# Kernel optimization log

Hardware: AMD Instinct MI355X
Metric: run time of the kernel (lower is better)

Reference implementation:

```python
import jax, jax.numpy as jnp
import numpy as np

GROUP = 64      # quantization group size along the K (in_features) dim
QMAX = 7.0      # symmetric signed int4 range [-7, 7]


def fake_quant_w4a4(t):
    """Per-group symmetric int4 fake-quantization along last dim (STE-friendly).

    t: [..., K] with K % GROUP == 0. Emulates nunchaku's quantize_w4a4
    numerics: scale = max|group| / 7, q = clip(round(t/scale)) * scale.
    """
    shp = t.shape
    g = t.reshape(shp[:-1] + (shp[-1] // GROUP, GROUP))
    scale = jnp.maximum(jnp.max(jnp.abs(g), axis=-1, keepdims=True) / QMAX, 1e-8)
    q = jnp.clip(jnp.round(g / scale), -QMAX, QMAX) * scale
    # straight-through estimator so gradients flow through the quant branch
    q = g + jax.lax.stop_gradient(q - g)
    return q.reshape(shp)


def setup_inputs() -> dict:
    key = jax.random.key(0)
    k0, k1, k2, k3, k4, k5 = jax.random.split(key, 6)
    B, K, N, R = 8192, 2048, 2048, 32  # tokens, in_features, out_features, rank
    x = jax.random.normal(k0, (B, K), jnp.float32)
    residual_weight = jax.random.normal(k1, (N, K), jnp.float32) * 0.02
    lora_down = jax.random.normal(k2, (K, R), jnp.float32) * 0.02
    lora_up = jax.random.normal(k3, (N, R), jnp.float32) * 0.02
    smooth = jax.random.uniform(k4, (K,), jnp.float32, minval=0.5, maxval=2.0)
    bias = jax.random.normal(k5, (N,), jnp.float32) * 0.01
    return {"x": x, "residual_weight": residual_weight, "lora_down": lora_down,
            "lora_up": lora_up, "smooth": smooth, "bias": bias}


def reference(x, residual_weight, lora_down, lora_up, smooth, bias):
    """SVDQuant forward: W4A4 GEMM on the residual weight fused with an
    FP low-rank (SVD) correction and per-channel smoothing.

    y = Q4(x*smooth) @ Q4(W_res).T + (x*smooth) @ lora_down @ lora_up.T + bias
    """
    x_s = x * smooth                                   # [B, K] smoothed activations
    y_lr = (x_s @ lora_down) @ lora_up.T               # [B, R] -> [B, N] low-rank branch
    y_q = fake_quant_w4a4(x_s) @ fake_quant_w4a4(residual_weight).T  # int4xint4 branch
    return y_q + y_lr + bias
```

## Files before the change

kernel.cpp:

```cpp
#include <hip/hip_runtime.h>
#include <stdint.h>


typedef __attribute__((ext_vector_type(8))) short short8;
typedef __attribute__((ext_vector_type(8))) unsigned short ushort8;
typedef __attribute__((ext_vector_type(4))) unsigned short ushort4v;
typedef __attribute__((ext_vector_type(4))) float floatx4;

#define M_TOK 8192
#define K_IN  2048
#define N_OUT 2048
#define RANK  32
#define KC    2112

__device__ __forceinline__ unsigned short f2bf(float f) {
  unsigned int u = __float_as_uint(f);
  u += 0x7fff + ((u >> 16) & 1);
  return (unsigned short)(u >> 16);
}

__global__ __launch_bounds__(256) void ldt_kernel(const float* __restrict__ ld,
                                                  unsigned short* __restrict__ ldT) {
  int i = blockIdx.x * 256 + threadIdx.x;
  int r = i >> 11;
  int k = i & 2047;
  ldT[r * K_IN + k] = f2bf(ld[k * RANK + r]);
}

__global__ __launch_bounds__(256) void quant_x_kernel(const float* __restrict__ x,
                                                      const float* __restrict__ smooth,
                                                      unsigned short* __restrict__ Xcat) {
  int row = blockIdx.x, tid = threadIdx.x;
  const float4* xr = (const float4*)(x + (size_t)row * K_IN);
  const float4* sr = (const float4*)smooth;
  float4 a0 = xr[tid * 2], a1 = xr[tid * 2 + 1];
  float4 s0 = sr[tid * 2], s1 = sr[tid * 2 + 1];
  float v[8] = {a0.x * s0.x, a0.y * s0.y, a0.z * s0.z, a0.w * s0.w,
                a1.x * s1.x, a1.y * s1.y, a1.z * s1.z, a1.w * s1.w};
  float amax = 0.f;
#pragma unroll
  for (int i = 0; i < 8; ++i) amax = fmaxf(amax, fabsf(v[i]));
  amax = fmaxf(amax, __shfl_xor(amax, 1, 64));
  amax = fmaxf(amax, __shfl_xor(amax, 2, 64));
  amax = fmaxf(amax, __shfl_xor(amax, 4, 64));
  float scale = fmaxf(amax / 7.0f, 1e-8f);
  ushort8 q;
#pragma unroll
  for (int i = 0; i < 8; ++i) {
    float qq = rintf(v[i] / scale);
    qq = fminf(fmaxf(qq, -7.f), 7.f);
    q[i] = f2bf(qq * scale);
  }
  *(ushort8*)(Xcat + (size_t)row * KC + tid * 8) = q;
  if (tid < 32) Xcat[(size_t)row * KC + 2080 + tid] = 0;
}

__global__ __launch_bounds__(256) void quant_w_kernel(const float* __restrict__ wgt,
                                                      const float* __restrict__ lup,
                                                      unsigned short* __restrict__ Wcat) {
  int row = blockIdx.x, tid = threadIdx.x;
  const float4* wr = (const float4*)(wgt + (size_t)row * K_IN);
  float4 a0 = wr[tid * 2], a1 = wr[tid * 2 + 1];
  float v[8] = {a0.x, a0.y, a0.z, a0.w, a1.x, a1.y, a1.z, a1.w};
  float amax = 0.f;
#pragma unroll
  for (int i = 0; i < 8; ++i) amax = fmaxf(amax, fabsf(v[i]));
  amax = fmaxf(amax, __shfl_xor(amax, 1, 64));
  amax = fmaxf(amax, __shfl_xor(amax, 2, 64));
  amax = fmaxf(amax, __shfl_xor(amax, 4, 64));
  float scale = fmaxf(amax / 7.0f, 1e-8f);
  ushort8 q;
#pragma unroll
  for (int i = 0; i < 8; ++i) {
    float qq = rintf(v[i] / scale);
    qq = fminf(fmaxf(qq, -7.f), 7.f);
    q[i] = f2bf(qq * scale);
  }
  *(ushort8*)(Wcat + (size_t)row * KC + tid * 8) = q;
  if (tid < 32)      Wcat[(size_t)row * KC + 2048 + tid] = f2bf(lup[row * RANK + tid]);
  else if (tid < 64) Wcat[(size_t)row * KC + 2048 + tid] = 0;
}

__global__ __launch_bounds__(256) void lowrank_kernel(const float* __restrict__ x,
                                                      const float* __restrict__ smooth,
                                                      const unsigned short* __restrict__ ldT,
                                                      unsigned short* __restrict__ Xcat) {
  __shared__ float red[4][16][32];
  int tid = threadIdx.x;
  int w = tid >> 6, lane = tid & 63, quad = lane >> 4, l16 = lane & 15;
  int rowbase = blockIdx.x * 16;
  floatx4 acc[2];
  acc[0] = (floatx4)0.f;
  acc[1] = (floatx4)0.f;
  int kbase = w * 512;
#pragma unroll 4
  for (int it = 0; it < 16; ++it) {
    int k = kbase + it * 32 + quad * 8;
    float4 sm0 = *(const float4*)(smooth + k);
    float4 sm1 = *(const float4*)(smooth + k + 4);
    short8 bfrag[2];
#pragma unroll
    for (int nt = 0; nt < 2; ++nt)
      bfrag[nt] = *(const short8*)(ldT + (size_t)(nt * 16 + l16) * K_IN + k);
    const float* xr = x + (size_t)(rowbase + l16) * K_IN + k;
    float4 x0 = *(const float4*)xr;
    float4 x1 = *(const float4*)(xr + 4);
    short8 af;
    af[0] = (short)f2bf(x0.x * sm0.x); af[1] = (short)f2bf(x0.y * sm0.y);
    af[2] = (short)f2bf(x0.z * sm0.z); af[3] = (short)f2bf(x0.w * sm0.w);
    af[4] = (short)f2bf(x1.x * sm1.x); af[5] = (short)f2bf(x1.y * sm1.y);
    af[6] = (short)f2bf(x1.z * sm1.z); af[7] = (short)f2bf(x1.w * sm1.w);
#pragma unroll
    for (int nt = 0; nt < 2; ++nt)
      acc[nt] = __builtin_amdgcn_mfma_f32_16x16x32_bf16(af, bfrag[nt], acc[nt], 0, 0, 0);
  }
#pragma unroll
  for (int nt = 0; nt < 2; ++nt)
#pragma unroll
    for (int r = 0; r < 4; ++r)
      red[w][quad * 4 + r][nt * 16 + l16] = acc[nt][r];
  __syncthreads();
  if (tid < 128) {
    int rl = tid >> 3, seg = tid & 7;
    ushort4v o;
#pragma unroll
    for (int j = 0; j < 4; ++j) {
      int c = seg * 4 + j;
      float s = red[0][rl][c] + red[1][rl][c] + red[2][rl][c] + red[3][rl][c];
      o[j] = f2bf(s);
    }
    *(ushort4v*)(Xcat + (size_t)(rowbase + rl) * KC + 2048 + seg * 4) = o;
  }
}

__device__ __forceinline__ void gld_lds16(const unsigned short* g, unsigned short* l) {
  __builtin_amdgcn_global_load_lds(
      (const __attribute__((address_space(1))) unsigned int*)g,
      (__attribute__((address_space(3))) unsigned int*)l, 16, 0, 0);
}

__global__ __launch_bounds__(256) void gemm_kernel(const unsigned short* __restrict__ Xcat,
                                                   const unsigned short* __restrict__ Wcat,
                                                   const float* __restrict__ bias,
                                                   float* __restrict__ out) {
  __shared__ unsigned short smem[16384];
  unsigned short* smemA = smem;
  unsigned short* smemB = smem + 8192;
  int tid = threadIdx.x;
  int w = tid >> 6, lane = tid & 63, quad = lane >> 4, l16 = lane & 15;
  int wm = w >> 1, wn = w & 1;
  int bM = blockIdx.y * 128, bN = blockIdx.x * 128;

  int srow = tid >> 3;
  int cs = (tid & 7) ^ (srow & 7);
  const unsigned short* Ag = Xcat + (size_t)(bM + srow) * KC + cs * 8;
  const unsigned short* Bg = Wcat + (size_t)(bN + srow) * KC + cs * 8;

  int c0 = (quad ^ (l16 & 7)) * 8;
  int c1 = ((4 + quad) ^ (l16 & 7)) * 8;
  int arow[4], brow[4];
#pragma unroll
  for (int mt = 0; mt < 4; ++mt) arow[mt] = (wm * 64 + mt * 16 + l16) * 64;
#pragma unroll
  for (int nt = 0; nt < 4; ++nt) brow[nt] = (wn * 64 + nt * 16 + l16) * 64;

  floatx4 acc[4][4];
#pragma unroll
  for (int mt = 0; mt < 4; ++mt)
#pragma unroll
    for (int nt = 0; nt < 4; ++nt) acc[mt][nt] = (floatx4)0.f;

  for (int kt = 0; kt < 33; ++kt) {
    int k0 = kt * 64;
#pragma unroll
    for (int rd = 0; rd < 4; ++rd) {
      gld_lds16(Ag + (size_t)rd * 32 * KC + k0, smemA + rd * 2048 + w * 512);
      gld_lds16(Bg + (size_t)rd * 32 * KC + k0, smemB + rd * 2048 + w * 512);
    }
    __syncthreads();

    short8 af[4][2], bf[4][2];
#pragma unroll
    for (int mt = 0; mt < 4; ++mt) {
      af[mt][0] = *(const short8*)(smemA + arow[mt] + c0);
      af[mt][1] = *(const short8*)(smemA + arow[mt] + c1);
    }
#pragma unroll
    for (int nt = 0; nt < 4; ++nt) {
      bf[nt][0] = *(const short8*)(smemB + brow[nt] + c0);
      bf[nt][1] = *(const short8*)(smemB + brow[nt] + c1);
    }
#pragma unroll
    for (int kb = 0; kb < 2; ++kb)
#pragma unroll
      for (int mt = 0; mt < 4; ++mt)
#pragma unroll
        for (int nt = 0; nt < 4; ++nt)
          acc[mt][nt] = __builtin_amdgcn_mfma_f32_16x16x32_bf16(af[mt][kb], bf[nt][kb],
                                                                acc[mt][nt], 0, 0, 0);
    __syncthreads();
  }

#pragma unroll
  for (int nt = 0; nt < 4; ++nt) {
    int col = bN + wn * 64 + nt * 16 + l16;
    float bv = bias[col];
#pragma unroll
    for (int mt = 0; mt < 4; ++mt) {
      int row = bM + wm * 64 + mt * 16 + quad * 4;
#pragma unroll
      for (int r = 0; r < 4; ++r)
        out[(size_t)(row + r) * N_OUT + col] = acc[mt][nt][r] + bv;
    }
  }
}

extern "C" void kernel_launch(void* const* d_in, const int* in_sizes, int n_in,
                              void* d_out, int out_size, void* d_ws, size_t ws_size,
                              hipStream_t stream) {
  const float* x      = (const float*)d_in[0];
  const float* wgt    = (const float*)d_in[1];
  const float* ld     = (const float*)d_in[2];
  const float* lup    = (const float*)d_in[3];
  const float* smooth = (const float*)d_in[4];
  const float* bias   = (const float*)d_in[5];
  float* out = (float*)d_out;

  unsigned short* Xcat = (unsigned short*)d_ws;
  unsigned short* Wcat = Xcat + (size_t)M_TOK * KC;
  unsigned short* ldT  = Wcat + (size_t)N_OUT * KC;

  hipLaunchKernelGGL(ldt_kernel,     dim3(256),    dim3(256), 0, stream, ld, ldT);
  hipLaunchKernelGGL(quant_x_kernel, dim3(M_TOK),  dim3(256), 0, stream, x, smooth, Xcat);
  hipLaunchKernelGGL(quant_w_kernel, dim3(N_OUT),  dim3(256), 0, stream, wgt, lup, Wcat);
  hipLaunchKernelGGL(lowrank_kernel, dim3(M_TOK/16), dim3(256), 0, stream, x, smooth, ldT, Xcat);
  hipLaunchKernelGGL(gemm_kernel,    dim3(N_OUT/128, M_TOK/128), dim3(256), 0, stream,
                     Xcat, Wcat, bias, out);
}
```

Before: 239.0 us.

## Fuse activation quantization with low-rank projection and merge weight prep kernels

Merges the ldT transpose into the weight quantization kernel and fuses activation quantization with the low-rank down-projection, so x is read from global memory once. The smoothed activations are staged as bf16 in a large shared buffer and reused for the MFMA low-rank step. This cuts kernel launches and one full pass over x, but the shared buffer (~66KB per block) limits occupancy, and each thread now holds a 64-float register array.

```diff
diff --git a/kernel.cpp b/kernel.cpp
--- a/kernel.cpp
+++ b/kernel.cpp
@@ -12,6 +12,7 @@
 #define N_OUT 2048
 #define RANK  32
 #define KC    2112
+#define XS_STRIDE 2056
 
 __device__ __forceinline__ unsigned short f2bf(float f) {
   unsigned int u = __float_as_uint(f);
@@ -19,24 +20,15 @@
   return (unsigned short)(u >> 16);
 }
 
-__global__ __launch_bounds__(256) void ldt_kernel(const float* __restrict__ ld,
-                                                  unsigned short* __restrict__ ldT) {
-  int i = blockIdx.x * 256 + threadIdx.x;
-  int r = i >> 11;
-  int k = i & 2047;
-  ldT[r * K_IN + k] = f2bf(ld[k * RANK + r]);
-}
-
-__global__ __launch_bounds__(256) void quant_x_kernel(const float* __restrict__ x,
-                                                      const float* __restrict__ smooth,
-                                                      unsigned short* __restrict__ Xcat) {
+__global__ __launch_bounds__(256) void wq_kernel(const float* __restrict__ wgt,
+                                                 const float* __restrict__ lup,
+                                                 const float* __restrict__ ld,
+                                                 unsigned short* __restrict__ Wcat,
+                                                 unsigned short* __restrict__ ldT) {
   int row = blockIdx.x, tid = threadIdx.x;
-  const float4* xr = (const float4*)(x + (size_t)row * K_IN);
-  const float4* sr = (const float4*)smooth;
-  float4 a0 = xr[tid * 2], a1 = xr[tid * 2 + 1];
-  float4 s0 = sr[tid * 2], s1 = sr[tid * 2 + 1];
-  float v[8] = {a0.x * s0.x, a0.y * s0.y, a0.z * s0.z, a0.w * s0.w,
-                a1.x * s1.x, a1.y * s1.y, a1.z * s1.z, a1.w * s1.w};
+  const float4* wr = (const float4*)(wgt + (size_t)row * K_IN);
+  float4 a0 = wr[tid * 2], a1 = wr[tid * 2 + 1];
+  float v[8] = {a0.x, a0.y, a0.z, a0.w, a1.x, a1.y, a1.z, a1.w};
   float amax = 0.f;
 #pragma unroll
   for (int i = 0; i < 8; ++i) amax = fmaxf(amax, fabsf(v[i]));
@@ -51,44 +43,66 @@
     qq = fminf(fmaxf(qq, -7.f), 7.f);
     q[i] = f2bf(qq * scale);
   }
-  *(ushort8*)(Xcat + (size_t)row * KC + tid * 8) = q;
-  if (tid < 32) Xcat[(size_t)row * KC + 2080 + tid] = 0;
-}
-
-__global__ __launch_bounds__(256) void quant_w_kernel(const float* __restrict__ wgt,
-                                                      const float* __restrict__ lup,
-                                                      unsigned short* __restrict__ Wcat) {
-  int row = blockIdx.x, tid = threadIdx.x;
-  const float4* wr = (const float4*)(wgt + (size_t)row * K_IN);
-  float4 a0 = wr[tid * 2], a1 = wr[tid * 2 + 1];
-  float v[8] = {a0.x, a0.y, a0.z, a0.w, a1.x, a1.y, a1.z, a1.w};
-  float amax = 0.f;
-#pragma unroll
-  for (int i = 0; i < 8; ++i) amax = fmaxf(amax, fabsf(v[i]));
-  amax = fmaxf(amax, __shfl_xor(amax, 1, 64));
-  amax = fmaxf(amax, __shfl_xor(amax, 2, 64));
-  amax = fmaxf(amax, __shfl_xor(amax, 4, 64));
-  float scale = fmaxf(amax / 7.0f, 1e-8f);
-  ushort8 q;
-#pragma unroll
-  for (int i = 0; i < 8; ++i) {
-    float qq = rintf(v[i] / scale);
-    qq = fminf(fmaxf(qq, -7.f), 7.f);
-    q[i] = f2bf(qq * scale);
-  }
   *(ushort8*)(Wcat + (size_t)row * KC + tid * 8) = q;
   if (tid < 32)      Wcat[(size_t)row * KC + 2048 + tid] = f2bf(lup[row * RANK + tid]);
   else if (tid < 64) Wcat[(size_t)row * KC + 2048 + tid] = 0;
-}
-
-__global__ __launch_bounds__(256) void lowrank_kernel(const float* __restrict__ x,
-                                                      const float* __restrict__ smooth,
-                                                      const unsigned short* __restrict__ ldT,
-                                                      unsigned short* __restrict__ Xcat) {
+  if (row < 256) {
+    int i = row * 256 + tid;
+    int r = i >> 11, k = i & 2047;
+    ldT[r * K_IN + k] = f2bf(ld[k * RANK + r]);
+  }
+}
+
+__global__ __launch_bounds__(256) void xq_kernel(const float* __restrict__ x,
+                                                 const float* __restrict__ smooth,
+                                                 const unsigned short* __restrict__ ldT,
+                                                 unsigned short* __restrict__ Xcat) {
+  __shared__ unsigned short xs[16 * XS_STRIDE];
   __shared__ float red[4][16][32];
   int tid = threadIdx.x;
   int w = tid >> 6, lane = tid & 63, quad = lane >> 4, l16 = lane & 15;
   int rowbase = blockIdx.x * 16;
+
+  {
+    int r = tid >> 4, seg = tid & 15;
+    const float4* xr = (const float4*)(x + (size_t)(rowbase + r) * K_IN + seg * 128);
+    const float4* sr = (const float4*)(smooth + seg * 128);
+    unsigned short* xc = Xcat + (size_t)(rowbase + r) * KC + seg * 128;
+    unsigned short* xl = xs + r * XS_STRIDE + seg * 128;
+#pragma unroll
+    for (int g = 0; g < 2; ++g) {
+      float v[64];
+      float amax = 0.f;
+#pragma unroll
+      for (int j = 0; j < 16; ++j) {
+        float4 a = xr[g * 16 + j];
+        float4 s = sr[g * 16 + j];
+        v[j * 4 + 0] = a.x * s.x; v[j * 4 + 1] = a.y * s.y;
+        v[j * 4 + 2] = a.z * s.z; v[j * 4 + 3] = a.w * s.w;
+        amax = fmaxf(amax, fmaxf(fmaxf(fabsf(v[j * 4]), fabsf(v[j * 4 + 1])),
+                                 fmaxf(fabsf(v[j * 4 + 2]), fabsf(v[j * 4 + 3]))));
+      }
+      float scale = fmaxf(amax / 7.0f, 1e-8f);
+#pragma unroll
+      for (int j = 0; j < 8; ++j) {
+        ushort8 q;
+#pragma unroll
+        for (int t = 0; t < 8; ++t) {
+          float qq = rintf(v[j * 8 + t] / scale);
+          qq = fminf(fmaxf(qq, -7.f), 7.f);
+          q[t] = f2bf(qq * scale);
+        }
+        *(ushort8*)(xc + g * 64 + j * 8) = q;
+        ushort8 sb;
+#pragma unroll
+        for (int t = 0; t < 8; ++t) sb[t] = f2bf(v[j * 8 + t]);
+        *(ushort8*)(xl + g * 64 + j * 8) = sb;
+      }
+    }
+    *(unsigned int*)(Xcat + (size_t)(rowbase + r) * KC + 2080 + seg * 2) = 0u;
+  }
+  __syncthreads();
+
   floatx4 acc[2];
   acc[0] = (floatx4)0.f;
   acc[1] = (floatx4)0.f;
@@ -96,23 +110,11 @@
 #pragma unroll 4
   for (int it = 0; it < 16; ++it) {
     int k = kbase + it * 32 + quad * 8;
-    float4 sm0 = *(const float4*)(smooth + k);
-    float4 sm1 = *(const float4*)(smooth + k + 4);
-    short8 bfrag[2];
-#pragma unroll
-    for (int nt = 0; nt < 2; ++nt)
-      bfrag[nt] = *(const short8*)(ldT + (size_t)(nt * 16 + l16) * K_IN + k);
-    const float* xr = x + (size_t)(rowbase + l16) * K_IN + k;
-    float4 x0 = *(const float4*)xr;
-    float4 x1 = *(const float4*)(xr + 4);
-    short8 af;
-    af[0] = (short)f2bf(x0.x * sm0.x); af[1] = (short)f2bf(x0.y * sm0.y);
-    af[2] = (short)f2bf(x0.z * sm0.z); af[3] = (short)f2bf(x0.w * sm0.w);
-    af[4] = (short)f2bf(x1.x * sm1.x); af[5] = (short)f2bf(x1.y * sm1.y);
-    af[6] = (short)f2bf(x1.z * sm1.z); af[7] = (short)f2bf(x1.w * sm1.w);
-#pragma unroll
-    for (int nt = 0; nt < 2; ++nt)
-      acc[nt] = __builtin_amdgcn_mfma_f32_16x16x32_bf16(af, bfrag[nt], acc[nt], 0, 0, 0);
+    short8 af = *(const short8*)(xs + l16 * XS_STRIDE + k);
+    short8 b0 = *(const short8*)(ldT + (size_t)l16 * K_IN + k);
+    short8 b1 = *(const short8*)(ldT + (size_t)(16 + l16) * K_IN + k);
+    acc[0] = __builtin_amdgcn_mfma_f32_16x16x32_bf16(af, b0, acc[0], 0, 0, 0);
+    acc[1] = __builtin_amdgcn_mfma_f32_16x16x32_bf16(af, b1, acc[1], 0, 0, 0);
   }
 #pragma unroll
   for (int nt = 0; nt < 2; ++nt)
@@ -230,10 +232,8 @@
   unsigned short* Wcat = Xcat + (size_t)M_TOK * KC;
   unsigned short* ldT  = Wcat + (size_t)N_OUT * KC;
 
-  hipLaunchKernelGGL(ldt_kernel,     dim3(256),    dim3(256), 0, stream, ld, ldT);
-  hipLaunchKernelGGL(quant_x_kernel, dim3(M_TOK),  dim3(256), 0, stream, x, smooth, Xcat);
-  hipLaunchKernelGGL(quant_w_kernel, dim3(N_OUT),  dim3(256), 0, stream, wgt, lup, Wcat);
-  hipLaunchKernelGGL(lowrank_kernel, dim3(M_TOK/16), dim3(256), 0, stream, x, smooth, ldT, Xcat);
-  hipLaunchKernelGGL(gemm_kernel,    dim3(N_OUT/128, M_TOK/128), dim3(256), 0, stream,
+  hipLaunchKernelGGL(wq_kernel,   dim3(N_OUT),    dim3(256), 0, stream, wgt, lup, ld, Wcat, ldT);
+  hipLaunchKernelGGL(xq_kernel,   dim3(M_TOK/16), dim3(256), 0, stream, x, smooth, ldT, Xcat);
+  hipLaunchKernelGGL(gemm_kernel, dim3(N_OUT/128, M_TOK/128), dim3(256), 0, stream,
                      Xcat, Wcat, bias, out);
 }
```

New measurement: 243.9 us. 1.02x slower.
